# Optimization experiments

Hardware: AMD Instinct MI355X
Metric: run time of the kernel (lower is better)

Reference implementation:

```python
import jax, jax.numpy as jnp
import numpy as np
from jax import lax

DIMS, IN_DIM, NW = 32, 32, 8
N, T, H, W = 8, 16, 112, 112
EPS = 1e-5

def setup_inputs() -> dict:
    key = jax.random.key(0)
    ks = jax.random.split(key, 12)
    fan = IN_DIM * 27
    inp = {
        'x': jax.random.normal(ks[0], (N, IN_DIM, T, H, W), jnp.float32),
        'std_x': jax.random.normal(ks[1], (N, 1, 32, 32), jnp.float32),
        'epochs_num': 5,
        'weights': jax.random.normal(ks[2], (NW, DIMS, IN_DIM, 3, 3, 3), jnp.float32) * np.sqrt(2.0 / fan),
        'biases': jax.random.normal(ks[3], (NW, DIMS), jnp.float32),
        'conv1_w': jax.random.normal(ks[4], (16, 1, 5, 5), jnp.float32) * 0.2,
        'conv1_b': jax.random.normal(ks[5], (16,), jnp.float32) * 0.1,
        'conv2_w': jax.random.normal(ks[6], (32, 16, 5, 5), jnp.float32) * 0.05,
        'conv2_b': jax.random.normal(ks[7], (32,), jnp.float32) * 0.1,
        'fc_w': jax.random.normal(ks[8], (NW, 32), jnp.float32) * 0.1,
        'fc_b': jax.random.normal(ks[9], (NW,), jnp.float32) * 0.1,
        'bn_gamma': jnp.ones((DIMS,), jnp.float32),
        'bn_beta': jnp.zeros((DIMS,), jnp.float32),
    }
    return inp

def _routing(std_x, c1w, c1b, c2w, c2b, fcw, fcb, tau):
    dn = ('NCHW', 'OIHW', 'NCHW')
    h = lax.conv_general_dilated(std_x, c1w, (1, 1), 'VALID', dimension_numbers=dn)
    h = jax.nn.relu(h + c1b[None, :, None, None])
    h = lax.conv_general_dilated(h, c2w, (1, 1), 'VALID', dimension_numbers=dn)
    h = jax.nn.relu(h + c2b[None, :, None, None])
    h = jnp.max(h, axis=(2, 3))                      # adaptive max pool to 1 -> [n,32]
    logits = h @ fcw.T + fcb                          # [n, num_weights]
    return jax.nn.softmax(logits / tau, axis=1)

def reference(x, std_x, epochs_num, weights, biases, conv1_w, conv1_b, conv2_w, conv2_b, fc_w, fc_b, bn_gamma, bn_beta):
    tau = 30.0 - 2.9 * epochs_num if epochs_num < 10 else 1.0
    phi = _routing(std_x, conv1_w, conv1_b, conv2_w, conv2_b, fc_w, fc_b, tau)
    dyn_w = jnp.einsum('bn,ncidhw->bcidhw', phi, weights)   # per-sample filters [n,dims,in,3,3,3]
    dyn_b = jnp.einsum('bn,nc->bc', phi, biases)            # [n,dims]
    dn3 = ('NCDHW', 'OIDHW', 'NCDHW')
    def per_sample(xi, wi):
        return lax.conv_general_dilated(xi[None], wi, (1, 1, 1), 'SAME', dimension_numbers=dn3)[0]
    y = jax.vmap(per_sample)(x, dyn_w)                      # [n,dims,T,H,W]
    y = y + dyn_b[:, :, None, None, None]
    # BatchNorm3d (training mode: batch stats, biased variance)
    mean = jnp.mean(y, axis=(0, 2, 3, 4))
    var = jnp.var(y, axis=(0, 2, 3, 4))
    y = (y - mean[None, :, None, None, None]) * lax.rsqrt(var + EPS)[None, :, None, None, None]
    y = y * bn_gamma[None, :, None, None, None] + bn_beta[None, :, None, None, None]
    return jax.nn.relu(y)
```

## Files before the change

### kernel.cpp

```cpp
#include <hip/hip_runtime.h>
#include <hip/hip_bf16.h>

#define IN_DIM 32
#define DIMS   32
#define NW     8
#define NB     8
#define TT     16
#define HH     112
#define WW     112
#define HW     (HH*WW)
#define CHW    (TT*HW)
#define EPS    1e-5f

typedef __attribute__((ext_vector_type(8))) short bf16x8;
typedef __attribute__((ext_vector_type(4))) float f32x4;

static __device__ __forceinline__ unsigned short f2bf(float f) {
    unsigned u = __float_as_uint(f);
    unsigned r = u + 0x7FFFu + ((u >> 16) & 1u);
    return (unsigned short)(r >> 16);
}

static __device__ __forceinline__ void gload_lds16(const void* gptr, void* lptr) {
    __builtin_amdgcn_global_load_lds(
        (const __attribute__((address_space(1))) unsigned int*)gptr,
        (__attribute__((address_space(3))) unsigned int*)lptr,
        16, 0, 0);
}

#define WSF_PHI    0
#define WSF_DYNB   64
#define WSF_STATS  320
#define WSF_ZERO   384
#define WSF_HDR_FLOATS 448
#define XT_USHORTS  ((size_t)NB*CHW*32)
#define WS_NEED_BYTES (WSF_HDR_FLOATS*4 + (size_t)NB*27*1024*2 + XT_USHORTS*2)

#define WS_PHI    0
#define WS_DYNW   64
#define WS_DYNB   221248
#define WS_STATS  221504
#define WS_SS     221568

__global__ __launch_bounds__(256)
void routing_conv1_kernel(const float* __restrict__ std_x,
                          const float* __restrict__ c1w, const float* __restrict__ c1b,
                          float* __restrict__ h1g)
{
    const int oc = blockIdx.x, b = blockIdx.y;
    const int tid = threadIdx.x;
    __shared__ float sx[1024];
    for (int i = tid; i < 1024; i += 256) sx[i] = std_x[b * 1024 + i];
    __syncthreads();

    float wloc[25];
    #pragma unroll
    for (int k = 0; k < 25; ++k) wloc[k] = c1w[oc * 25 + k];
    const float bias = c1b[oc];

    for (int idx = tid; idx < 784; idx += 256) {
        int xw = idx % 28, xh = idx / 28;
        float s = bias;
        #pragma unroll
        for (int ky = 0; ky < 5; ++ky)
            #pragma unroll
            for (int kx = 0; kx < 5; ++kx)
                s = fmaf(sx[(xh + ky) * 32 + xw + kx], wloc[ky * 5 + kx], s);
        h1g[(b * 16 + oc) * 784 + idx] = fmaxf(s, 0.f);
    }
}

__global__ __launch_bounds__(256)
void routing_conv2max_kernel(const float* __restrict__ h1g,
                             const float* __restrict__ c2w, const float* __restrict__ c2b,
                             float* __restrict__ cmax)
{
    const int oc = blockIdx.x, b = blockIdx.y;
    const int tid = threadIdx.x;
    __shared__ float h1s[16 * 784];
    __shared__ float wred[4];

    for (int i = tid; i < 16 * 784; i += 256) h1s[i] = h1g[b * (16 * 784) + i];
    __syncthreads();

    float m = 0.f;
    for (int idx = tid; idx < 576; idx += 256) {
        int xw = idx % 24, xh = idx / 24;
        float s = c2b[oc];
        for (int ic = 0; ic < 16; ++ic) {
            const float* hp = &h1s[ic * 784];
            const float* wp = &c2w[(oc * 16 + ic) * 25];
            #pragma unroll
            for (int ky = 0; ky < 5; ++ky)
                #pragma unroll
                for (int kx = 0; kx < 5; ++kx)
                    s = fmaf(hp[(xh + ky) * 28 + xw + kx], wp[ky * 5 + kx], s);
        }
        m = fmaxf(m, s);
    }
    #pragma unroll
    for (int off = 32; off >= 1; off >>= 1) m = fmaxf(m, __shfl_down(m, off));
    if ((tid & 63) == 0) wred[tid >> 6] = m;
    __syncthreads();
    if (tid == 0) {
        float r = fmaxf(fmaxf(wred[0], wred[1]), fmaxf(wred[2], wred[3]));
        cmax[b * 32 + oc] = r;
    }
}

__global__ __launch_bounds__(64)
void routing_fc_kernel(const float* __restrict__ cmax, const int* __restrict__ epochs,
                       const float* __restrict__ fcw, const float* __restrict__ fcb,
                       float* __restrict__ phi_out)
{
    const int tid = threadIdx.x;
    const int b = tid >> 3, n = tid & 7;
    int ep = epochs[0];
    float tau = (ep < 10) ? (30.0f - 2.9f * (float)ep) : 1.0f;
    float s = fcb[n];
    #pragma unroll
    for (int k = 0; k < 32; ++k) s = fmaf(cmax[b * 32 + k], fcw[n * 32 + k], s);
    s /= tau;
    float mx = s;
    #pragma unroll
    for (int off = 1; off < 8; off <<= 1) mx = fmaxf(mx, __shfl_xor(mx, off, 8));
    float e = expf(s - mx);
    float den = e;
    #pragma unroll
    for (int off = 1; off < 8; off <<= 1) den += __shfl_xor(den, off, 8);
    phi_out[b * 8 + n] = e / den;
}

#define XS 232
__global__ __launch_bounds__(256)
void xpose_kernel(const float* __restrict__ x, unsigned short* __restrict__ xT)
{
    const int h = blockIdx.x, t = blockIdx.y, b = blockIdx.z;
    const int tid = threadIdx.x;
    __shared__ __align__(16) unsigned char lds[32 * XS];

    for (int idx = tid; idx < 32 * 28; idx += 256) {
        int ic = idx / 28;
        int w4 = idx - ic * 28;
        const float4 v = *(const float4*)(x + (((size_t)(b * 32 + ic) * TT + t) * HW) + h * 112 + w4 * 4);
        uint2 pk;
        pk.x = (unsigned)f2bf(v.x) | ((unsigned)f2bf(v.y) << 16);
        pk.y = (unsigned)f2bf(v.z) | ((unsigned)f2bf(v.w) << 16);
        *(uint2*)(lds + ic * XS + w4 * 8) = pk;
    }
    __syncthreads();

    unsigned short* op = xT + ((((size_t)b * TT + t) * HH + h) * WW) * 32;
    for (int idx = tid; idx < 448; idx += 256) {
        int w = idx >> 2, icg = idx & 3;
        unsigned int pk[4];
        #pragma unroll
        for (int j = 0; j < 4; ++j) {
            unsigned short lo = *(unsigned short*)(lds + (icg * 8 + 2 * j) * XS + w * 2);
            unsigned short hi = *(unsigned short*)(lds + (icg * 8 + 2 * j + 1) * XS + w * 2);
            pk[j] = (unsigned int)lo | ((unsigned int)hi << 16);
        }
        uint4 v; v.x = pk[0]; v.y = pk[1]; v.z = pk[2]; v.w = pk[3];
        *(uint4*)(op + (size_t)w * 32 + icg * 8) = v;
    }
}

__global__ __launch_bounds__(256)
void dynwb_kernel(const float* __restrict__ phi, const float* __restrict__ weights,
                  const float* __restrict__ biases, unsigned short* __restrict__ dwb,
                  float* __restrict__ dyn_b, float* __restrict__ statszero)
{
    const int oc = blockIdx.x;
    const int b  = blockIdx.y;
    const int tid = threadIdx.x;
    __shared__ float ph[8];
    if (tid < 8) ph[tid] = phi[b * 8 + tid];
    __syncthreads();

    for (int i = tid; i < 864; i += 256) {
        float s = 0.f;
        #pragma unroll
        for (int n = 0; n < 8; ++n)
            s = fmaf(ph[n], weights[(size_t)(n * 32 + oc) * 864 + i], s);
        int ic = i / 27;
        int tap = i - 27 * ic;
        dwb[((size_t)(b * 27 + tap) << 10) + (oc << 5) + ic] = f2bf(s);
    }
    if (tid == 0) {
        float s = 0.f;
        #pragma unroll
        for (int n = 0; n < 8; ++n) s = fmaf(ph[n], biases[n * 32 + oc], s);
        dyn_b[b * 32 + oc] = s;
    }
    if (oc == 0 && b == 0 && tid < 128) statszero[tid] = 0.f;
}

#define ROWSTRIDE   (18 * 64)
#define CELLS       1296
#define BUF_BYTES   (1536 * 16)
#define PLANE_BYTES_G 802816ull
__global__ __launch_bounds__(256, 3)
void convmf_kernel(const unsigned short* __restrict__ xT, const unsigned short* __restrict__ dwb,
                   const float* __restrict__ dyn_b, const float* __restrict__ zerobuf,
                   float* __restrict__ y, float* __restrict__ stats)
{
    const int hblk = blockIdx.x / 7, wblk = blockIdx.x % 7;
    const int tpair = blockIdx.y, b = blockIdx.z;
    const int h0 = hblk * 16, w0 = wblk * 16, t0 = tpair * 2;
    const int tid = threadIdx.x;
    const int lane = tid & 63, wv = tid >> 6;
    const int l15 = lane & 15, lg = lane >> 4;

    __shared__ __align__(16) unsigned char ldsx[2 * BUF_BYTES];
    __shared__ float sred[4][64];

    const unsigned char* xTbase = (const unsigned char*)xT + (size_t)b * TT * PLANE_BYTES_G;
    const unsigned char* zbp = (const unsigned char*)zerobuf;
    const unsigned char* cb[6];
    bool okhw[6];
    #pragma unroll
    for (int j = 0; j < 6; ++j) {
        int cid = j * 256 + tid;
        int hr = cid / 72, rem = cid - hr * 72;
        int p = rem >> 2, icg = rem & 3;
        int gh = h0 - 1 + hr, gw = w0 - 1 + p;
        okhw[j] = (cid < CELLS) && ((unsigned)gh < (unsigned)HH) && ((unsigned)gw < (unsigned)WW);
        cb[j] = xTbase + (ptrdiff_t)(gh * WW + gw) * 64 + icg * 16;
    }
    unsigned char* lwave = ldsx + (size_t)(tid & ~63) * 16;

#define STAGE(TX, SEL) do {                                                   \
        const int tx_ = (TX);                                                 \
        const bool tok_ = ((unsigned)tx_ < (unsigned)TT);                     \
        const size_t toff_ = (size_t)tx_ * PLANE_BYTES_G;                     \
        unsigned char* lb_ = lwave + (SEL) * BUF_BYTES;                       \
        _Pragma("unroll")                                                     \
        for (int j = 0; j < 6; ++j) {                                         \
            const unsigned char* s_ = (tok_ && okhw[j]) ? cb[j] + toff_ : zbp;\
            gload_lds16(s_, lb_ + j * 4096);                                  \
        }                                                                     \
    } while (0)

    f32x4 acc0[4][2], acc1[4][2];
    #pragma unroll
    for (int g = 0; g < 4; ++g)
        #pragma unroll
        for (int M = 0; M < 2; ++M) { acc0[g][M] = (f32x4)0.f; acc1[g][M] = (f32x4)0.f; }

    const unsigned short* wbase = dwb + (size_t)b * 27 * 1024;

    STAGE(t0 - 1, 0);
    asm volatile("s_waitcnt vmcnt(0)" ::: "memory");
    __syncthreads();

    #pragma unroll
    for (int tp = 0; tp < 4; ++tp) {
        const bool do0 = (tp <= 2), do1 = (tp >= 1);
        const int dt0 = tp, dt1 = tp - 1;
        const unsigned char* ldsp = ldsx + (tp & 1) * BUF_BYTES;

        #pragma unroll
        for (int dhw = 0; dhw < 9; ++dhw) {
            const int dh = dhw / 3, dw = dhw - dh * 3;
            bf16x8 a00, a01, a10, a11;
            if (do0) {
                const unsigned short* wp = wbase + (dt0 * 9 + dhw) * 1024 + l15 * 32 + lg * 8;
                a00 = *(const bf16x8*)(wp);
                a01 = *(const bf16x8*)(wp + 512);
            }
            if (do1) {
                const unsigned short* wp = wbase + (dt1 * 9 + dhw) * 1024 + l15 * 32 + lg * 8;
                a10 = *(const bf16x8*)(wp);
                a11 = *(const bf16x8*)(wp + 512);
            }
            const unsigned char* bb0 = ldsp + (wv * 4 + dh) * ROWSTRIDE + (l15 + dw) * 64 + lg * 16;
            #pragma unroll
            for (int g = 0; g < 4; ++g) {
                bf16x8 bb = *(const bf16x8*)(bb0 + g * ROWSTRIDE);
                if (do0) {
                    acc0[g][0] = __builtin_amdgcn_mfma_f32_16x16x32_bf16(a00, bb, acc0[g][0], 0, 0, 0);
                    acc0[g][1] = __builtin_amdgcn_mfma_f32_16x16x32_bf16(a01, bb, acc0[g][1], 0, 0, 0);
                }
                if (do1) {
                    acc1[g][0] = __builtin_amdgcn_mfma_f32_16x16x32_bf16(a10, bb, acc1[g][0], 0, 0, 0);
                    acc1[g][1] = __builtin_amdgcn_mfma_f32_16x16x32_bf16(a11, bb, acc1[g][1], 0, 0, 0);
                }
            }
        }

        if (tp < 3) STAGE(t0 + tp, (tp + 1) & 1);

        asm volatile("s_waitcnt vmcnt(0)" ::: "memory");
        __syncthreads();
    }
#undef STAGE

    f32x4 bias[2];
    #pragma unroll
    for (int M = 0; M < 2; ++M)
        #pragma unroll
        for (int r = 0; r < 4; ++r)
            bias[M][r] = dyn_b[b * 32 + 16 * M + lg * 4 + r];

    float sumv[2][4], sqv[2][4];
    #pragma unroll
    for (int M = 0; M < 2; ++M)
        #pragma unroll
        for (int r = 0; r < 4; ++r) { sumv[M][r] = 0.f; sqv[M][r] = 0.f; }

    #pragma unroll
    for (int g = 0; g < 4; ++g) {
        const int h = h0 + wv * 4 + g;
        #pragma unroll
        for (int M = 0; M < 2; ++M) {
            f32x4 v0 = acc0[g][M] + bias[M];
            f32x4 v1 = acc1[g][M] + bias[M];
            const int oc0 = 16 * M + lg * 4;
            size_t base = (((size_t)(b * 32 + oc0) * TT + t0) * HW) + h * 112 + w0 + l15;
            #pragma unroll
            for (int r = 0; r < 4; ++r) {
                sumv[M][r] += v0[r] + v1[r];
                sqv[M][r]  += v0[r] * v0[r] + v1[r] * v1[r];
                y[base + (size_t)r * TT * HW] = v0[r];
                y[base + (size_t)r * TT * HW + HW] = v1[r];
            }
        }
    }

    #pragma unroll
    for (int off = 1; off < 16; off <<= 1) {
        #pragma unroll
        for (int M = 0; M < 2; ++M)
            #pragma unroll
            for (int r = 0; r < 4; ++r) {
                sumv[M][r] += __shfl_xor(sumv[M][r], off);
                sqv[M][r]  += __shfl_xor(sqv[M][r], off);
            }
    }
    if (l15 == 0) {
        #pragma unroll
        for (int M = 0; M < 2; ++M)
            #pragma unroll
            for (int r = 0; r < 4; ++r) {
                int ch = 16 * M + lg * 4 + r;
                sred[wv][ch] = sumv[M][r];
                sred[wv][32 + ch] = sqv[M][r];
            }
    }
    __syncthreads();
    if (tid < 64) {
        float v = sred[0][tid] + sred[1][tid] + sred[2][tid] + sred[3][tid];
        atomicAdd(&stats[tid], v);
    }
}

__global__ __launch_bounds__(256)
void norm_relu_fused_kernel(float* __restrict__ y, const float* __restrict__ stats,
                            const float* __restrict__ gamma, const float* __restrict__ beta)
{
    __shared__ float ssc[32], ssh[32];
    if (threadIdx.x < 32) {
        int c = threadIdx.x;
        const float M = (float)NB * (float)CHW;
        float mean = stats[c] / M;
        float var  = stats[32 + c] / M - mean * mean;
        float sc = gamma[c] * rsqrtf(var + EPS);
        ssc[c] = sc;
        ssh[c] = beta[c] - mean * sc;
    }
    __syncthreads();

    const long long total4 = (long long)NB * DIMS * CHW / 4;
    const int nthreads = gridDim.x * blockDim.x;
    float4* y4 = reinterpret_cast<float4*>(y);
    for (long long i = (long long)blockIdx.x * blockDim.x + threadIdx.x; i < total4; i += nthreads) {
        int c = (int)((i / (CHW / 4)) & 31);
        float sc = ssc[c];
        float sh = ssh[c];
        float4 v = y4[i];
        v.x = fmaxf(fmaf(v.x, sc, sh), 0.f);
        v.y = fmaxf(fmaf(v.y, sc, sh), 0.f);
        v.z = fmaxf(fmaf(v.z, sc, sh), 0.f);
        v.w = fmaxf(fmaf(v.w, sc, sh), 0.f);
        y4[i] = v;
    }
}

__global__ __launch_bounds__(256)
void routing_kernel(const float* __restrict__ std_x, const int* __restrict__ epochs,
                    const float* __restrict__ c1w, const float* __restrict__ c1b,
                    const float* __restrict__ c2w, const float* __restrict__ c2b,
                    const float* __restrict__ fcw, const float* __restrict__ fcb,
                    float* __restrict__ phi_out)
{
    const int b = blockIdx.x;
    const int tid = threadIdx.x;
    __shared__ float sx[32 * 32];
    __shared__ float h1[16 * 28 * 28];
    __shared__ float cmax[32];

    for (int i = tid; i < 1024; i += 256) sx[i] = std_x[b * 1024 + i];
    if (tid < 32) cmax[tid] = 0.f;
    __syncthreads();

    for (int idx = tid; idx < 16 * 28 * 28; idx += 256) {
        int xw = idx % 28;
        int r = idx / 28;
        int xh = r % 28;
        int oc = r / 28;
        float s = c1b[oc];
        #pragma unroll
        for (int ky = 0; ky < 5; ++ky)
            #pragma unroll
            for (int kx = 0; kx < 5; ++kx)
                s = fmaf(sx[(xh + ky) * 32 + xw + kx], c1w[oc * 25 + ky * 5 + kx], s);
        h1[idx] = fmaxf(s, 0.f);
    }
    __syncthreads();

    for (int idx = tid; idx < 32 * 24 * 24; idx += 256) {
        int xw = idx % 24;
        int r = idx / 24;
        int xh = r % 24;
        int oc = r / 24;
        float s = c2b[oc];
        for (int ic = 0; ic < 16; ++ic) {
            const float* hp = &h1[ic * 784];
            const float* wp = &c2w[(oc * 16 + ic) * 25];
            #pragma unroll
            for (int ky = 0; ky < 5; ++ky)
                #pragma unroll
                for (int kx = 0; kx < 5; ++kx)
                    s = fmaf(hp[(xh + ky) * 28 + xw + kx], wp[ky * 5 + kx], s);
        }
        s = fmaxf(s, 0.f);
        atomicMax(reinterpret_cast<int*>(&cmax[oc]), __float_as_int(s));
    }
    __syncthreads();

    if (tid == 0) {
        int ep = epochs[0];
        float tau = (ep < 10) ? (30.0f - 2.9f * (float)ep) : 1.0f;
        float lg[8];
        float mx = -1e30f;
        #pragma unroll
        for (int n = 0; n < 8; ++n) {
            float s = fcb[n];
            #pragma unroll
            for (int k = 0; k < 32; ++k) s = fmaf(cmax[k], fcw[n * 32 + k], s);
            lg[n] = s / tau;
            mx = fmaxf(mx, lg[n]);
        }
        float den = 0.f;
        #pragma unroll
        for (int n = 0; n < 8; ++n) { lg[n] = expf(lg[n] - mx); den += lg[n]; }
        #pragma unroll
        for (int n = 0; n < 8; ++n) phi_out[b * 8 + n] = lg[n] / den;
    }
}

__global__ __launch_bounds__(256)
void dynw_kernel(const float* __restrict__ phi, const float* __restrict__ weights,
                 const float* __restrict__ biases, float* __restrict__ dyn_w,
                 float* __restrict__ dyn_b, float* __restrict__ stats)
{
    const int b = blockIdx.x;
    const int tid = threadIdx.x;
    __shared__ float ph[8];
    if (tid < 8) ph[tid] = phi[b * 8 + tid];
    __syncthreads();

    for (int j = tid; j < DIMS * IN_DIM * 27; j += 256) {
        float s = 0.f;
        #pragma unroll
        for (int n = 0; n < 8; ++n) s = fmaf(ph[n], weights[n * (DIMS * IN_DIM * 27) + j], s);
        dyn_w[b * (DIMS * IN_DIM * 27) + j] = s;
    }
    if (tid < 32) {
        float s = 0.f;
        #pragma unroll
        for (int n = 0; n < 8; ++n) s = fmaf(ph[n], biases[n * 32 + tid], s);
        dyn_b[b * 32 + tid] = s;
    }
    if (b == 0 && tid < 64) stats[tid] = 0.f;
}

__global__ __launch_bounds__(256)
void conv3d_kernel(const float* __restrict__ x, const float* __restrict__ dyn_w,
                   const float* __restrict__ dyn_b, float* __restrict__ y,
                   float* __restrict__ stats)
{
    const int htile = blockIdx.x;
    const int t     = blockIdx.y;
    const int b     = blockIdx.z;
    const int tid   = threadIdx.x;
    const int w     = tid & 127;
    const int hh    = tid >> 7;
    const int h0    = htile * 2;

    __shared__ float tile[3][8][4][114];

    float acc[32];
    #pragma unroll
    for (int c = 0; c < 32; ++c) acc[c] = 0.f;

    const float* wb = dyn_w + b * (DIMS * IN_DIM * 27);
    const float* xb = x + (size_t)b * IN_DIM * CHW;

    for (int ic0 = 0; ic0 < 32; ic0 += 8) {
        __syncthreads();
        for (int idx = tid; idx < 3 * 8 * 4 * 114; idx += 256) {
            int w_ = idx % 114;
            int r  = idx / 114;
            int h_ = r & 3;
            int r2 = r >> 2;
            int i_ = r2 & 7;
            int dt_ = r2 >> 3;
            int gt = t + dt_ - 1;
            int gh = h0 - 1 + h_;
            int gw = w_ - 1;
            float v = 0.f;
            if ((unsigned)gt < (unsigned)TT && (unsigned)gh < (unsigned)HH && (unsigned)gw < (unsigned)WW)
                v = xb[(size_t)((ic0 + i_) * TT + gt) * HW + gh * WW + gw];
            tile[dt_][i_][h_][w_] = v;
        }
        __syncthreads();

        if (w < WW) {
            for (int i = 0; i < 8; ++i) {
                #pragma unroll
                for (int dt = 0; dt < 3; ++dt) {
                    float xv[9];
                    #pragma unroll
                    for (int dh = 0; dh < 3; ++dh)
                        #pragma unroll
                        for (int dw = 0; dw < 3; ++dw)
                            xv[dh * 3 + dw] = tile[dt][i][hh + dh][w + dw];
                    const float* wp = wb + (ic0 + i) * 27 + dt * 9;
                    #pragma unroll
                    for (int c = 0; c < 32; ++c) {
                        const float* wc = wp + c * 864;
                        #pragma unroll
                        for (int k = 0; k < 9; ++k)
                            acc[c] = fmaf(xv[k], wc[k], acc[c]);
                    }
                }
            }
        }
    }

    const float* db = dyn_b + b * 32;
    if (w < WW) {
        #pragma unroll
        for (int c = 0; c < 32; ++c) acc[c] += db[c];
    }

    __shared__ float ssum[32], ssq[32];
    if (tid < 32) { ssum[tid] = 0.f; ssq[tid] = 0.f; }
    __syncthreads();
    #pragma unroll
    for (int c = 0; c < 32; ++c) {
        float s = (w < WW) ? acc[c] : 0.f;
        float q = s * s;
        #pragma unroll
        for (int off = 32; off >= 1; off >>= 1) {
            s += __shfl_down(s, off);
            q += __shfl_down(q, off);
        }
        if ((tid & 63) == 0) { atomicAdd(&ssum[c], s); atomicAdd(&ssq[c], q); }
    }
    __syncthreads();
    if (tid < 32) {
        atomicAdd(&stats[tid], ssum[tid]);
        atomicAdd(&stats[32 + tid], ssq[tid]);
    }

    if (w < WW) {
        size_t base = ((size_t)(b * 32) * TT + t) * HW + (size_t)(h0 + hh) * WW + w;
        #pragma unroll
        for (int c = 0; c < 32; ++c)
            y[base + (size_t)c * CHW] = acc[c];
    }
}

__global__ void stats_finalize_kernel(const float* __restrict__ stats,
                                      const float* __restrict__ gamma,
                                      const float* __restrict__ beta,
                                      float* __restrict__ scaleshift)
{
    int c = threadIdx.x;
    const float M = (float)NB * (float)CHW;
    float mean = stats[c] / M;
    float var  = stats[32 + c] / M - mean * mean;
    float sc = gamma[c] * rsqrtf(var + EPS);
    scaleshift[c] = sc;
    scaleshift[32 + c] = beta[c] - mean * sc;
}

__global__ __launch_bounds__(256)
void norm_relu_kernel(float* __restrict__ y, const float* __restrict__ scaleshift)
{
    const long long total4 = (long long)NB * DIMS * CHW / 4;
    const int nthreads = gridDim.x * blockDim.x;
    float4* y4 = reinterpret_cast<float4*>(y);
    for (long long i = (long long)blockIdx.x * blockDim.x + threadIdx.x; i < total4; i += nthreads) {
        int c = (int)((i / (CHW / 4)) & 31);
        float sc = scaleshift[c];
        float sh = scaleshift[32 + c];
        float4 v = y4[i];
        v.x = fmaxf(fmaf(v.x, sc, sh), 0.f);
        v.y = fmaxf(fmaf(v.y, sc, sh), 0.f);
        v.z = fmaxf(fmaf(v.z, sc, sh), 0.f);
        v.w = fmaxf(fmaf(v.w, sc, sh), 0.f);
        y4[i] = v;
    }
}

extern "C" void kernel_launch(void* const* d_in, const int* in_sizes, int n_in,
                              void* d_out, int out_size, void* d_ws, size_t ws_size,
                              hipStream_t stream)
{
    const float* x      = (const float*)d_in[0];
    const float* std_x  = (const float*)d_in[1];
    const int*   epochs = (const int*)d_in[2];
    const float* weights= (const float*)d_in[3];
    const float* biases = (const float*)d_in[4];
    const float* c1w    = (const float*)d_in[5];
    const float* c1b    = (const float*)d_in[6];
    const float* c2w    = (const float*)d_in[7];
    const float* c2b    = (const float*)d_in[8];
    const float* fcw    = (const float*)d_in[9];
    const float* fcb    = (const float*)d_in[10];
    const float* gamma  = (const float*)d_in[11];
    const float* beta   = (const float*)d_in[12];

    float* out = (float*)d_out;
    float* ws  = (float*)d_ws;

    if (ws_size >= WS_NEED_BYTES) {
        float* phi   = ws + WSF_PHI;
        float* dyn_b = ws + WSF_DYNB;
        float* stats = ws + WSF_STATS;
        float* zerob = ws + WSF_ZERO;
        unsigned short* dwb = (unsigned short*)(ws + WSF_HDR_FLOATS);
        unsigned short* xT  = dwb + (size_t)NB * 27 * 1024;
        float* h1g  = (float*)xT;
        float* cmax = h1g + NB * 16 * 784;

        routing_conv1_kernel<<<dim3(16, NB), 256, 0, stream>>>(std_x, c1w, c1b, h1g);
        routing_conv2max_kernel<<<dim3(32, NB), 256, 0, stream>>>(h1g, c2w, c2b, cmax);
        routing_fc_kernel<<<1, 64, 0, stream>>>(cmax, epochs, fcw, fcb, phi);
        dynwb_kernel<<<dim3(32, NB), 256, 0, stream>>>(phi, weights, biases, dwb, dyn_b, stats);
        xpose_kernel<<<dim3(HH, TT, NB), 256, 0, stream>>>(x, xT);
        convmf_kernel<<<dim3(49, 8, NB), 256, 0, stream>>>(xT, dwb, dyn_b, zerob, out, stats);
        norm_relu_fused_kernel<<<2048, 256, 0, stream>>>(out, stats, gamma, beta);
    } else {
        float* phi   = ws + WS_PHI;
        float* dyn_w = ws + WS_DYNW;
        float* dyn_b = ws + WS_DYNB;
        float* stats = ws + WS_STATS;
        float* ss    = ws + WS_SS;

        routing_kernel<<<NB, 256, 0, stream>>>(std_x, epochs, c1w, c1b, c2w, c2b, fcw, fcb, phi);
        dynw_kernel<<<NB, 256, 0, stream>>>(phi, weights, biases, dyn_w, dyn_b, stats);
        conv3d_kernel<<<dim3(HH / 2, TT, NB), 256, 0, stream>>>(x, dyn_w, dyn_b, out, stats);
        stats_finalize_kernel<<<1, 32, 0, stream>>>(stats, gamma, beta, ss);
        norm_relu_kernel<<<2048, 256, 0, stream>>>(out, ss);
    }
}
```

Before: 634.1 us.

## Stage conv weights in LDS and swizzle input tile via register prefetch

The 3D conv kernel now copies all 27 weight taps for its sample into LDS once, replacing per-iteration global loads of the A operands. The input plane staging moves from double-buffered direct global-to-LDS loads to register prefetch followed by a single-buffered LDS write with an XOR swizzle meant to avoid bank conflicts. The larger LDS footprint lowers the occupancy bound from 3 to 2 blocks per CU, and the extra barrier per time step adds sync overhead.

```diff
diff --git a/kernel.cpp b/kernel.cpp
--- a/kernel.cpp
+++ b/kernel.cpp
@@ -195,14 +195,14 @@
     if (oc == 0 && b == 0 && tid < 128) statszero[tid] = 0.f;
 }
 
-#define ROWSTRIDE   (18 * 64)
-#define CELLS       1296
-#define BUF_BYTES   (1536 * 16)
+#define XROWSTRIDE   1152
+#define XLDS_BYTES   20736
+#define WLDS_BYTES   55296
 #define PLANE_BYTES_G 802816ull
-__global__ __launch_bounds__(256, 3)
+__global__ __launch_bounds__(256, 2)
 void convmf_kernel(const unsigned short* __restrict__ xT, const unsigned short* __restrict__ dwb,
-                   const float* __restrict__ dyn_b, const float* __restrict__ zerobuf,
-                   float* __restrict__ y, float* __restrict__ stats)
+                   const float* __restrict__ dyn_b, float* __restrict__ y,
+                   float* __restrict__ stats)
 {
     const int hblk = blockIdx.x / 7, wblk = blockIdx.x % 7;
     const int tpair = blockIdx.y, b = blockIdx.z;
@@ -211,72 +211,103 @@
     const int lane = tid & 63, wv = tid >> 6;
     const int l15 = lane & 15, lg = lane >> 4;
 
-    __shared__ __align__(16) unsigned char ldsx[2 * BUF_BYTES];
+    __shared__ __align__(16) unsigned char wlds[WLDS_BYTES];
+    __shared__ __align__(16) unsigned char xlds[XLDS_BYTES];
     __shared__ float sred[4][64];
 
-    const unsigned char* xTbase = (const unsigned char*)xT + (size_t)b * TT * PLANE_BYTES_G;
-    const unsigned char* zbp = (const unsigned char*)zerobuf;
-    const unsigned char* cb[6];
-    bool okhw[6];
+    {
+        const unsigned short* wb = dwb + (size_t)b * 27 * 1024;
+        unsigned char* ldsw = wlds + (size_t)(tid & ~63) * 16;
+        #pragma unroll
+        for (int k = 0; k < 14; ++k) {
+            if (k < 13 || tid < 128) {
+                int cid = k * 256 + tid;
+                int tap = cid >> 7;
+                int rem = cid & 127;
+                int oc  = rem >> 2;
+                int icg_s = rem & 3;
+                int icg_l = icg_s ^ ((oc >> 1) & 3);
+                gload_lds16(wb + tap * 1024 + oc * 32 + icg_l * 8, ldsw + k * 4096);
+            }
+        }
+    }
+
+    const unsigned char* xbase = (const unsigned char*)xT + (size_t)b * TT * PLANE_BYTES_G;
+    int srcoff[6], dsto[6];
+    bool okj[6], valid[6];
     #pragma unroll
     for (int j = 0; j < 6; ++j) {
         int cid = j * 256 + tid;
         int hr = cid / 72, rem = cid - hr * 72;
         int p = rem >> 2, icg = rem & 3;
         int gh = h0 - 1 + hr, gw = w0 - 1 + p;
-        okhw[j] = (cid < CELLS) && ((unsigned)gh < (unsigned)HH) && ((unsigned)gw < (unsigned)WW);
-        cb[j] = xTbase + (ptrdiff_t)(gh * WW + gw) * 64 + icg * 16;
-    }
-    unsigned char* lwave = ldsx + (size_t)(tid & ~63) * 16;
-
-#define STAGE(TX, SEL) do {                                                   \
+        valid[j] = (cid < 1296);
+        okj[j] = valid[j] && ((unsigned)gh < (unsigned)HH) && ((unsigned)gw < (unsigned)WW);
+        srcoff[j] = (gh * WW + gw) * 64 + icg * 16;
+        dsto[j] = (hr * 72 + p * 4 + (icg ^ ((p >> 1) & 3))) * 16;
+    }
+    uint4 xs[6];
+
+#define LOADX(TX) do {                                                        \
         const int tx_ = (TX);                                                 \
         const bool tok_ = ((unsigned)tx_ < (unsigned)TT);                     \
-        const size_t toff_ = (size_t)tx_ * PLANE_BYTES_G;                     \
-        unsigned char* lb_ = lwave + (SEL) * BUF_BYTES;                       \
+        const unsigned char* pb_ = xbase + (size_t)tx_ * PLANE_BYTES_G;       \
         _Pragma("unroll")                                                     \
         for (int j = 0; j < 6; ++j) {                                         \
-            const unsigned char* s_ = (tok_ && okhw[j]) ? cb[j] + toff_ : zbp;\
-            gload_lds16(s_, lb_ + j * 4096);                                  \
+            uint4 v_; v_.x = 0; v_.y = 0; v_.z = 0; v_.w = 0;                 \
+            if (tok_ && okj[j]) v_ = *(const uint4*)(pb_ + srcoff[j]);        \
+            xs[j] = v_;                                                       \
         }                                                                     \
     } while (0)
 
+#define WRITEX() do {                                                         \
+        _Pragma("unroll")                                                     \
+        for (int j = 0; j < 6; ++j)                                           \
+            if (valid[j]) *(uint4*)(xlds + dsto[j]) = xs[j];                  \
+    } while (0)
+
+    const int wsw = l15 * 64 + ((lg ^ ((l15 >> 1) & 3)) * 16);
+    int xoff[3];
+    #pragma unroll
+    for (int dw = 0; dw < 3; ++dw) {
+        int px = l15 + dw;
+        xoff[dw] = px * 64 + ((lg ^ ((px >> 1) & 3)) * 16);
+    }
+
     f32x4 acc0[4][2], acc1[4][2];
     #pragma unroll
     for (int g = 0; g < 4; ++g)
         #pragma unroll
         for (int M = 0; M < 2; ++M) { acc0[g][M] = (f32x4)0.f; acc1[g][M] = (f32x4)0.f; }
 
-    const unsigned short* wbase = dwb + (size_t)b * 27 * 1024;
-
-    STAGE(t0 - 1, 0);
+    LOADX(t0 - 1);
     asm volatile("s_waitcnt vmcnt(0)" ::: "memory");
+    WRITEX();
     __syncthreads();
 
     #pragma unroll
     for (int tp = 0; tp < 4; ++tp) {
+        if (tp < 3) LOADX(t0 + tp);
+
         const bool do0 = (tp <= 2), do1 = (tp >= 1);
-        const int dt0 = tp, dt1 = tp - 1;
-        const unsigned char* ldsp = ldsx + (tp & 1) * BUF_BYTES;
-
         #pragma unroll
         for (int dhw = 0; dhw < 9; ++dhw) {
             const int dh = dhw / 3, dw = dhw - dh * 3;
             bf16x8 a00, a01, a10, a11;
             if (do0) {
-                const unsigned short* wp = wbase + (dt0 * 9 + dhw) * 1024 + l15 * 32 + lg * 8;
-                a00 = *(const bf16x8*)(wp);
-                a01 = *(const bf16x8*)(wp + 512);
+                const int off = (tp * 9 + dhw) * 2048 + wsw;
+                a00 = *(const bf16x8*)(wlds + off);
+                a01 = *(const bf16x8*)(wlds + off + 1024);
             }
             if (do1) {
-                const unsigned short* wp = wbase + (dt1 * 9 + dhw) * 1024 + l15 * 32 + lg * 8;
-                a10 = *(const bf16x8*)(wp);
-                a11 = *(const bf16x8*)(wp + 512);
+                const int off = ((tp - 1) * 9 + dhw) * 2048 + wsw;
+                a10 = *(const bf16x8*)(wlds + off);
+                a11 = *(const bf16x8*)(wlds + off + 1024);
             }
-            const unsigned char* bb0 = ldsp + (wv * 4 + dh) * ROWSTRIDE + (l15 + dw) * 64 + lg * 16;
+            const int rb = wv * 4 + dh;
             #pragma unroll
             for (int g = 0; g < 4; ++g) {
-                bf16x8 bb = *(const bf16x8*)(bb0 + g * ROWSTRIDE);
+                bf16x8 bb = *(const bf16x8*)(xlds + (rb + g) * XROWSTRIDE + xoff[dw]);
                 if (do0) {
                     acc0[g][0] = __builtin_amdgcn_mfma_f32_16x16x32_bf16(a00, bb, acc0[g][0], 0, 0, 0);
                     acc0[g][1] = __builtin_amdgcn_mfma_f32_16x16x32_bf16(a01, bb, acc0[g][1], 0, 0, 0);
@@ -288,12 +319,15 @@
             }
         }
 
-        if (tp < 3) STAGE(t0 + tp, (tp + 1) & 1);
-
-        asm volatile("s_waitcnt vmcnt(0)" ::: "memory");
-        __syncthreads();
-    }
-#undef STAGE
+        if (tp < 3) {
+            __syncthreads();
+            asm volatile("s_waitcnt vmcnt(0)" ::: "memory");
+            WRITEX();
+            __syncthreads();
+        }
+    }
+#undef LOADX
+#undef WRITEX
 
     f32x4 bias[2];
     #pragma unroll
@@ -641,7 +675,6 @@
         float* phi   = ws + WSF_PHI;
         float* dyn_b = ws + WSF_DYNB;
         float* stats = ws + WSF_STATS;
-        float* zerob = ws + WSF_ZERO;
         unsigned short* dwb = (unsigned short*)(ws + WSF_HDR_FLOATS);
         unsigned short* xT  = dwb + (size_t)NB * 27 * 1024;
         float* h1g  = (float*)xT;
@@ -652,7 +685,7 @@
         routing_fc_kernel<<<1, 64, 0, stream>>>(cmax, epochs, fcw, fcb, phi);
         dynwb_kernel<<<dim3(32, NB), 256, 0, stream>>>(phi, weights, biases, dwb, dyn_b, stats);
         xpose_kernel<<<dim3(HH, TT, NB), 256, 0, stream>>>(x, xT);
-        convmf_kernel<<<dim3(49, 8, NB), 256, 0, stream>>>(xT, dwb, dyn_b, zerob, out, stats);
+        convmf_kernel<<<dim3(49, 8, NB), 256, 0, stream>>>(xT, dwb, dyn_b, out, stats);
         norm_relu_fused_kernel<<<2048, 256, 0, stream>>>(out, stats, gamma, beta);
     } else {
         float* phi   = ws + WS_PHI;
```

Result: faster. 571.0 us (-9.9%).
